# Optimization experiments

Measured on AMD Instinct MI355X. Metric: run time of the kernel, lower is better.

## Reference

```python
import jax, jax.numpy as jnp
import numpy as np

HIDDEN = 128
LR = 0.01          # epsilon (energy optimizer Adam lr)
B1, B2, EPS = 0.9, 0.999, 1e-8  # torch.optim.Adam defaults


def rho(s):
    return jnp.clip(s, 0.0, 1.0)


def setup_inputs() -> dict:
    key = jax.random.key(0)
    k_x, k_w0, k_w1 = jax.random.split(key, 3)
    input_size, output_size = 262144, 1024
    x = jax.random.uniform(k_x, (input_size,), dtype=jnp.float32)
    # xavier_uniform as in nn.init.xavier_uniform_
    lim0 = float(np.sqrt(6.0 / (input_size + HIDDEN)))
    W0 = jax.random.uniform(k_w0, (input_size, HIDDEN), jnp.float32, -lim0, lim0)
    lim1 = float(np.sqrt(6.0 / (HIDDEN + output_size)))
    W1 = jax.random.uniform(k_w1, (HIDDEN, output_size), jnp.float32, -lim1, lim1)
    b0 = jnp.zeros((input_size,), jnp.float32)
    b1 = jnp.zeros((HIDDEN,), jnp.float32)
    b2 = jnp.zeros((output_size,), jnp.float32)
    return {"x": x, "b0": b0, "b1": b1, "b2": b2, "W0": W0, "W1": W1,
            "n_iterations": 20}


def reference(x, b0, b1, b2, W0, W1, n_iterations):
    # Energy: sum ||rho(layer)||^2/2 - sum rho(layer).b - sum rho(pre) W rho(post)
    def energy(h, o):
        rx, rh, ro = rho(x), rho(h), rho(o)
        sq = 0.5 * (rx @ rx + rh @ rh + ro @ ro)
        lin = -(rx @ b0 + rh @ b1 + ro @ b2)
        quad = -((rx @ W0) @ rh + (rh @ W1) @ ro)
        return sq + lin + quad

    grad_e = jax.grad(energy, argnums=(0, 1))

    def adam_update(s, m, v, g, t):
        m = B1 * m + (1.0 - B1) * g
        v = B2 * v + (1.0 - B2) * (g * g)
        m_hat = m / (1.0 - jnp.power(jnp.float32(B1), t))
        v_hat = v / (1.0 - jnp.power(jnp.float32(B2), t))
        s = s - LR * m_hat / (jnp.sqrt(v_hat) + EPS)
        return s, m, v

    def step(carry, _):
        h, o, mh, vh, mo, vo, t = carry
        t = t + 1.0
        gh, go = grad_e(h, o)
        h, mh, vh = adam_update(h, mh, vh, gh, t)
        o, mo, vo = adam_update(o, mo, vo, go, t)
        return (h, o, mh, vh, mo, vo, t), None

    z_h = jnp.zeros_like(b1)  # hidden state starts at zeros
    z_o = jnp.zeros_like(b2)  # output state starts at zeros
    carry0 = (z_h, z_o, z_h, z_h, z_o, z_o, jnp.float32(0.0))
    (h, o, *_), _ = jax.lax.scan(step, carry0, None, length=int(n_iterations))
    return o
```

## Files before the change

### kernel.cpp

```cpp
#include <hip/hip_runtime.h>
#include <math.h>

#define NBLK_B 8

__device__ __forceinline__ float rho(float s) {
  return fminf(fmaxf(s, 0.0f), 1.0f);
}

__device__ __forceinline__ float drho(float s) {
  if (s < 0.0f || s > 1.0f) return 0.0f;
  float g = 1.0f;
  if (s == 0.0f) g *= 0.5f;
  if (s == 1.0f) g *= 0.5f;
  return g;
}

template <int ROWS>
__global__ __launch_bounds__(256) void k1_xw0(const float* __restrict__ x,
                                              const float* __restrict__ W0,
                                              float* __restrict__ part,
                                              int* __restrict__ flags) {
  __shared__ float xs[ROWS];
  __shared__ float red[8][132];
  const int t = threadIdx.x;
  const int b = blockIdx.x;
  if (b == 0 && t < NBLK_B) flags[t * 32] = 0;
  const int r0 = b * ROWS;
  for (int i = t; i < ROWS; i += 256) xs[i] = rho(x[r0 + i]);
  __syncthreads();
  const int cq = t & 31;
  const int rg = t >> 5;
  constexpr int GR = ROWS / 8;
  const float4* __restrict__ W4 = reinterpret_cast<const float4*>(W0);
  float ax = 0.f, ay = 0.f, az = 0.f, aw = 0.f;
  const int base = (r0 + rg * GR) * 32 + cq;
#pragma unroll 8
  for (int i = 0; i < GR; ++i) {
    const float xv = xs[rg * GR + i];
    const float4 w = W4[base + i * 32];
    ax = fmaf(xv, w.x, ax);
    ay = fmaf(xv, w.y, ay);
    az = fmaf(xv, w.z, az);
    aw = fmaf(xv, w.w, aw);
  }
  red[rg][cq * 4 + 0] = ax;
  red[rg][cq * 4 + 1] = ay;
  red[rg][cq * 4 + 2] = az;
  red[rg][cq * 4 + 3] = aw;
  __syncthreads();
  if (t < 128) {
    float s = 0.f;
#pragma unroll
    for (int g = 0; g < 8; ++g) s += red[g][t];
    part[b * 128 + t] = s;
  }
}

__global__ __launch_bounds__(256) void k1b_reduce(const float* __restrict__ part1,
                                                  float* __restrict__ part2) {
  __shared__ float acc[2][128];
  const int t = threadIdx.x, i = blockIdx.x;
  const int jk = t & 127, half = t >> 7;
  float s = 0.f;
  const int r0 = i * 32 + half * 16;
#pragma unroll
  for (int r = 0; r < 16; ++r) s += part1[(r0 + r) * 128 + jk];
  acc[half][jk] = s;
  __syncthreads();
  if (half == 0) part2[i * 128 + jk] = acc[0][jk] + acc[1][jk];
}

__global__ __launch_bounds__(256) void k2_iter(const float* __restrict__ part2,
                                               const int npart2,
                                               const float* __restrict__ W1,
                                               const float* __restrict__ b1,
                                               const float* __restrict__ b2,
                                               const int* __restrict__ niterp,
                                               float* __restrict__ aPartG,
                                               int* __restrict__ flags,
                                               float* __restrict__ out) {
  __shared__ float w1s[128 * 128];
  __shared__ float rhs_[128];
  __shared__ float ros_[128];
  __shared__ float c0s[128];
  __shared__ float b1s[128];
  __shared__ float bpart[2][128];
  __shared__ float apl[2][128];

  const int t = threadIdx.x;
  const int p = blockIdx.x;
  const int jk = t & 127;
  const int half = t >> 7;

  const float4* __restrict__ W14 = reinterpret_cast<const float4*>(W1);
#pragma unroll
  for (int itr = 0; itr < 16; ++itr) {
    const int e4 = itr * 256 + t;
    const int j = e4 >> 5;
    const int c4 = e4 & 31;
    const float4 w = W14[j * 256 + p * 32 + c4];
    const int rb = j * 128;
    const int sw = j & 31;
    const int c = c4 * 4;
    w1s[rb + ((c + 0) ^ sw)] = w.x;
    w1s[rb + ((c + 1) ^ sw)] = w.y;
    w1s[rb + ((c + 2) ^ sw)] = w.z;
    w1s[rb + ((c + 3) ^ sw)] = w.w;
  }
  {
    float s = 0.f;
#pragma unroll 8
    for (int r = half; r < npart2; r += 2) s += part2[r * 128 + jk];
    bpart[half][jk] = s;
  }
  const int niter = *niterp;
  const float b2v = (half == 0) ? b2[p * 128 + jk] : 0.f;
  __syncthreads();
  if (half == 0) {
    c0s[jk] = bpart[0][jk] + bpart[1][jk];
    b1s[jk] = b1[jk];
    rhs_[jk] = 0.f;
    ros_[jk] = 0.f;
    __hip_atomic_store(&aPartG[1 * 1024 + p * 128 + jk], 0.f,
                       __ATOMIC_RELAXED, __HIP_MEMORY_SCOPE_AGENT);
  }
  __syncthreads();
  if (t == 0) {
    __threadfence();
    __hip_atomic_store(&flags[p * 32], 1, __ATOMIC_RELEASE,
                       __HIP_MEMORY_SCOPE_AGENT);
  }

  float hreg = 0.f, mh = 0.f, vh = 0.f;
  float oreg = 0.f, mo = 0.f, vo = 0.f;
  float p1 = 1.f, p2 = 1.f;
  const int x0 = half * 64;

  for (int it = 1; it <= niter; ++it) {
    p1 *= 0.9f;
    p2 *= 0.999f;
    const float bc1 = 1.0f - p1;
    const float bc2 = 1.0f - p2;
    if (t < NBLK_B) {
      while (__hip_atomic_load(&flags[t * 32], __ATOMIC_ACQUIRE,
                               __HIP_MEMORY_SCOPE_AGENT) < it)
        __builtin_amdgcn_s_sleep(1);
    }
    __syncthreads();
    float ga[NBLK_B];
    if (half == 0) {
      const int rslot = it & 3;
#pragma unroll
      for (int q = 0; q < NBLK_B; ++q)
        ga[q] = __hip_atomic_load(&aPartG[rslot * 1024 + q * 128 + jk],
                                  __ATOMIC_RELAXED, __HIP_MEMORY_SCOPE_AGENT);
    }
    {
      float a0 = 0.f, a1 = 0.f, a2 = 0.f, a3 = 0.f;
#pragma unroll
      for (int u = 0; u < 64; u += 4) {
        const int j0 = x0 + u;
        a0 = fmaf(rhs_[j0 + 0], w1s[(j0 + 0) * 128 + (jk ^ ((j0 + 0) & 31))], a0);
        a1 = fmaf(rhs_[j0 + 1], w1s[(j0 + 1) * 128 + (jk ^ ((j0 + 1) & 31))], a1);
        a2 = fmaf(rhs_[j0 + 2], w1s[(j0 + 2) * 128 + (jk ^ ((j0 + 2) & 31))], a2);
        a3 = fmaf(rhs_[j0 + 3], w1s[(j0 + 3) * 128 + (jk ^ ((j0 + 3) & 31))], a3);
      }
      bpart[half][jk] = (a0 + a1) + (a2 + a3);
    }
    __syncthreads();
    if (half == 0) {
      const float bsum = bpart[0][jk] + bpart[1][jk];
      const float rot = rho(oreg);
      const float go = drho(oreg) * (rot - b2v - bsum);
      mo = 0.9f * mo + 0.1f * go;
      vo = 0.999f * vo + 0.001f * (go * go);
      oreg = oreg - 0.01f * (mo / bc1) / (sqrtf(vo / bc2) + 1e-8f);
      ros_[jk] = rho(oreg);
    }
    __syncthreads();
    {
      float a0 = 0.f, a1 = 0.f, a2 = 0.f, a3 = 0.f;
#pragma unroll
      for (int u = 0; u < 64; u += 4) {
        const int c0i = x0 + u;
        a0 = fmaf(w1s[jk * 128 + ((c0i + 0) ^ (jk & 31))], ros_[c0i + 0], a0);
        a1 = fmaf(w1s[jk * 128 + ((c0i + 1) ^ (jk & 31))], ros_[c0i + 1], a1);
        a2 = fmaf(w1s[jk * 128 + ((c0i + 2) ^ (jk & 31))], ros_[c0i + 2], a2);
        a3 = fmaf(w1s[jk * 128 + ((c0i + 3) ^ (jk & 31))], ros_[c0i + 3], a3);
      }
      apl[half][jk] = (a0 + a1) + (a2 + a3);
    }
    __syncthreads();
    if (half == 0)
      __hip_atomic_store(&aPartG[((it + 1) & 3) * 1024 + p * 128 + jk],
                         apl[0][jk] + apl[1][jk], __ATOMIC_RELAXED,
                         __HIP_MEMORY_SCOPE_AGENT);
    __syncthreads();
    if (t == 0) {
      __threadfence();
      __hip_atomic_store(&flags[p * 32], it + 1, __ATOMIC_RELEASE,
                         __HIP_MEMORY_SCOPE_AGENT);
    }
    if (half == 0) {
      const float a = ((ga[0] + ga[1]) + (ga[2] + ga[3])) +
                      ((ga[4] + ga[5]) + (ga[6] + ga[7]));
      const float gh = drho(hreg) * (rhs_[jk] - b1s[jk] - c0s[jk] - a);
      mh = 0.9f * mh + 0.1f * gh;
      vh = 0.999f * vh + 0.001f * (gh * gh);
      hreg = hreg - 0.01f * (mh / bc1) / (sqrtf(vh / bc2) + 1e-8f);
      rhs_[jk] = rho(hreg);
    }
    __syncthreads();
  }
  if (half == 0) out[p * 128 + jk] = oreg;
}

extern "C" void kernel_launch(void* const* d_in, const int* in_sizes, int n_in,
                              void* d_out, int out_size, void* d_ws,
                              size_t ws_size, hipStream_t stream) {
  const float* x  = (const float*)d_in[0];
  const float* b1 = (const float*)d_in[2];
  const float* b2 = (const float*)d_in[3];
  const float* W0 = (const float*)d_in[4];
  const float* W1 = (const float*)d_in[5];
  const int*   ni = (const int*)d_in[6];
  float* out = (float*)d_out;

  char* ws = (char*)d_ws;
  int*   flags  = (int*)ws;
  float* aPartG = (float*)(ws + 1024);
  float* part2  = (float*)(ws + 1024 + 16384);
  float* part1  = (float*)(ws + 1024 + 16384 + 16384);

  const int nrows = in_sizes[0];
  const size_t hdr = 1024 + 16384 + 16384;
  int nblk1;
  if (ws_size >= hdr + (size_t)(nrows / 256) * 512) {
    nblk1 = nrows / 256;
    hipLaunchKernelGGL(k1_xw0<256>, dim3(nblk1), dim3(256), 0, stream,
                       x, W0, part1, flags);
  } else if (ws_size >= hdr + (size_t)(nrows / 512) * 512) {
    nblk1 = nrows / 512;
    hipLaunchKernelGGL(k1_xw0<512>, dim3(nblk1), dim3(256), 0, stream,
                       x, W0, part1, flags);
  } else {
    nblk1 = nrows / 1024;
    hipLaunchKernelGGL(k1_xw0<1024>, dim3(nblk1), dim3(256), 0, stream,
                       x, W0, part1, flags);
  }
  const int nblk2 = nblk1 / 32;
  hipLaunchKernelGGL(k1b_reduce, dim3(nblk2), dim3(256), 0, stream,
                     part1, part2);
  hipLaunchKernelGGL(k2_iter, dim3(NBLK_B), dim3(256), 0, stream,
                     part2, nblk2, W1, b1, b2, ni, aPartG, flags, out);
}
```

Measured before the change: 91.17 us.

## Co-locate iterative-phase blocks on one XCD via oversubscribed grid and role election

```diff
diff --git a/kernel.cpp b/kernel.cpp
--- a/kernel.cpp
+++ b/kernel.cpp
@@ -2,11 +2,11 @@
 #include <math.h>
 
 #define NBLK_B 8
+#define K2_GRID 128
 
 __device__ __forceinline__ float rho(float s) {
   return fminf(fmaxf(s, 0.0f), 1.0f);
 }
-
 __device__ __forceinline__ float drho(float s) {
   if (s < 0.0f || s > 1.0f) return 0.0f;
   float g = 1.0f;
@@ -19,12 +19,18 @@
 __global__ __launch_bounds__(256) void k1_xw0(const float* __restrict__ x,
                                               const float* __restrict__ W0,
                                               float* __restrict__ part,
-                                              int* __restrict__ flags) {
+                                              int* __restrict__ flags,
+                                              int* __restrict__ cnt,
+                                              int* __restrict__ chosen) {
   __shared__ float xs[ROWS];
   __shared__ float red[8][132];
   const int t = threadIdx.x;
   const int b = blockIdx.x;
-  if (b == 0 && t < NBLK_B) flags[t * 32] = 0;
+  if (b == 0) {
+    if (t < NBLK_B) flags[t * 32] = 0;
+    if (t >= 32 && t < 48) cnt[t - 32] = 0;
+    if (t == 48) *chosen = -1;
+  }
   const int r0 = b * ROWS;
   for (int i = t; i < ROWS; i += 256) xs[i] = rho(x[r0 + i]);
   __syncthreads();
@@ -78,6 +84,8 @@
                                                const int* __restrict__ niterp,
                                                float* __restrict__ aPartG,
                                                int* __restrict__ flags,
+                                               int* __restrict__ cnt,
+                                               int* __restrict__ chosen,
                                                float* __restrict__ out) {
   __shared__ float w1s[128 * 128];
   __shared__ float rhs_[128];
@@ -86,11 +94,33 @@
   __shared__ float b1s[128];
   __shared__ float bpart[2][128];
   __shared__ float apl[2][128];
+  __shared__ int role;
 
   const int t = threadIdx.x;
-  const int p = blockIdx.x;
   const int jk = t & 127;
   const int half = t >> 7;
+
+  if (t == 0) {
+    int xcc;
+    asm volatile("s_getreg_b32 %0, hwreg(HW_REG_XCC_ID)" : "=s"(xcc));
+    xcc &= 15;
+    const int r = __hip_atomic_fetch_add(&cnt[xcc], 1, __ATOMIC_RELAXED,
+                                         __HIP_MEMORY_SCOPE_AGENT);
+    if (r == NBLK_B - 1) {
+      int expected = -1;
+      __hip_atomic_compare_exchange_strong(chosen, &expected, xcc,
+                                           __ATOMIC_ACQ_REL, __ATOMIC_ACQUIRE,
+                                           __HIP_MEMORY_SCOPE_AGENT);
+    }
+    int ch;
+    while ((ch = __hip_atomic_load(chosen, __ATOMIC_ACQUIRE,
+                                   __HIP_MEMORY_SCOPE_AGENT)) < 0)
+      __builtin_amdgcn_s_sleep(8);
+    role = (ch == xcc && r < NBLK_B) ? r : -1;
+  }
+  __syncthreads();
+  const int p = role;
+  if (p < 0) return;
 
   const float4* __restrict__ W14 = reinterpret_cast<const float4*>(W1);
 #pragma unroll
@@ -108,10 +138,17 @@
     w1s[rb + ((c + 3) ^ sw)] = w.w;
   }
   {
-    float s = 0.f;
-#pragma unroll 8
-    for (int r = half; r < npart2; r += 2) s += part2[r * 128 + jk];
-    bpart[half][jk] = s;
+    const int n = npart2 >> 1;
+    const int base = half * n;
+    float s0 = 0.f, s1 = 0.f, s2 = 0.f, s3 = 0.f;
+#pragma unroll 4
+    for (int r = 0; r < n; r += 4) {
+      s0 += part2[(base + r + 0) * 128 + jk];
+      s1 += part2[(base + r + 1) * 128 + jk];
+      s2 += part2[(base + r + 2) * 128 + jk];
+      s3 += part2[(base + r + 3) * 128 + jk];
+    }
+    bpart[half][jk] = (s0 + s1) + (s2 + s3);
   }
   const int niter = *niterp;
   const float b2v = (half == 0) ? b2[p * 128 + jk] : 0.f;
@@ -133,14 +170,14 @@
 
   float hreg = 0.f, mh = 0.f, vh = 0.f;
   float oreg = 0.f, mo = 0.f, vo = 0.f;
-  float p1 = 1.f, p2 = 1.f;
+  float pw1 = 1.f, pw2 = 1.f;
   const int x0 = half * 64;
 
   for (int it = 1; it <= niter; ++it) {
-    p1 *= 0.9f;
-    p2 *= 0.999f;
-    const float bc1 = 1.0f - p1;
-    const float bc2 = 1.0f - p2;
+    pw1 *= 0.9f;
+    pw2 *= 0.999f;
+    const float bc1 = 1.0f - pw1;
+    const float bc2 = 1.0f - pw2;
     if (t < NBLK_B) {
       while (__hip_atomic_load(&flags[t * 32], __ATOMIC_ACQUIRE,
                                __HIP_MEMORY_SCOPE_AGENT) < it)
@@ -228,29 +265,32 @@
 
   char* ws = (char*)d_ws;
   int*   flags  = (int*)ws;
-  float* aPartG = (float*)(ws + 1024);
-  float* part2  = (float*)(ws + 1024 + 16384);
-  float* part1  = (float*)(ws + 1024 + 16384 + 16384);
+  int*   cnt    = (int*)(ws + 1024);
+  int*   chosen = (int*)(ws + 1152);
+  float* aPartG = (float*)(ws + 2048);
+  float* part2  = (float*)(ws + 18432);
+  float* part1  = (float*)(ws + 34816);
 
   const int nrows = in_sizes[0];
-  const size_t hdr = 1024 + 16384 + 16384;
+  const size_t hdr = 34816;
   int nblk1;
   if (ws_size >= hdr + (size_t)(nrows / 256) * 512) {
     nblk1 = nrows / 256;
     hipLaunchKernelGGL(k1_xw0<256>, dim3(nblk1), dim3(256), 0, stream,
-                       x, W0, part1, flags);
+                       x, W0, part1, flags, cnt, chosen);
   } else if (ws_size >= hdr + (size_t)(nrows / 512) * 512) {
     nblk1 = nrows / 512;
     hipLaunchKernelGGL(k1_xw0<512>, dim3(nblk1), dim3(256), 0, stream,
-                       x, W0, part1, flags);
+                       x, W0, part1, flags, cnt, chosen);
   } else {
     nblk1 = nrows / 1024;
     hipLaunchKernelGGL(k1_xw0<1024>, dim3(nblk1), dim3(256), 0, stream,
-                       x, W0, part1, flags);
+                       x, W0, part1, flags, cnt, chosen);
   }
   const int nblk2 = nblk1 / 32;
   hipLaunchKernelGGL(k1b_reduce, dim3(nblk2), dim3(256), 0, stream,
                      part1, part2);
-  hipLaunchKernelGGL(k2_iter, dim3(NBLK_B), dim3(256), 0, stream,
-                     part2, nblk2, W1, b1, b2, ni, aPartG, flags, out);
-}
+  hipLaunchKernelGGL(k2_iter, dim3(K2_GRID), dim3(256), 0, stream,
+                     part2, nblk2, W1, b1, b2, ni, aPartG, flags, cnt, chosen,
+                     out);
+}
```

Measured after the change: 98.88 us. +8.5%, slower.

## Replace flag-based inter-block barrier with per-element tagged 64-bit value slots

Applied to the files above, without the earlier changes.

```diff
diff --git a/kernel.cpp b/kernel.cpp
--- a/kernel.cpp
+++ b/kernel.cpp
@@ -6,7 +6,6 @@
 __device__ __forceinline__ float rho(float s) {
   return fminf(fmaxf(s, 0.0f), 1.0f);
 }
-
 __device__ __forceinline__ float drho(float s) {
   if (s < 0.0f || s > 1.0f) return 0.0f;
   float g = 1.0f;
@@ -19,12 +18,15 @@
 __global__ __launch_bounds__(256) void k1_xw0(const float* __restrict__ x,
                                               const float* __restrict__ W0,
                                               float* __restrict__ part,
-                                              int* __restrict__ flags) {
+                                              unsigned long long* __restrict__ aPartG) {
   __shared__ float xs[ROWS];
   __shared__ float red[8][132];
   const int t = threadIdx.x;
   const int b = blockIdx.x;
-  if (b == 0 && t < NBLK_B) flags[t * 32] = 0;
+  if (b == 0) {
+#pragma unroll
+    for (int i = 0; i < 16; ++i) aPartG[i * 256 + t] = 0ull;
+  }
   const int r0 = b * ROWS;
   for (int i = t; i < ROWS; i += 256) xs[i] = rho(x[r0 + i]);
   __syncthreads();
@@ -76,8 +78,7 @@
                                                const float* __restrict__ b1,
                                                const float* __restrict__ b2,
                                                const int* __restrict__ niterp,
-                                               float* __restrict__ aPartG,
-                                               int* __restrict__ flags,
+                                               unsigned long long* __restrict__ aPartG,
                                                float* __restrict__ out) {
   __shared__ float w1s[128 * 128];
   __shared__ float rhs_[128];
@@ -121,40 +122,21 @@
     b1s[jk] = b1[jk];
     rhs_[jk] = 0.f;
     ros_[jk] = 0.f;
-    __hip_atomic_store(&aPartG[1 * 1024 + p * 128 + jk], 0.f,
+    __hip_atomic_store(&aPartG[1 * 1024 + jk * 8 + p], 1ull << 32,
                        __ATOMIC_RELAXED, __HIP_MEMORY_SCOPE_AGENT);
   }
   __syncthreads();
-  if (t == 0) {
-    __threadfence();
-    __hip_atomic_store(&flags[p * 32], 1, __ATOMIC_RELEASE,
-                       __HIP_MEMORY_SCOPE_AGENT);
-  }
 
   float hreg = 0.f, mh = 0.f, vh = 0.f;
   float oreg = 0.f, mo = 0.f, vo = 0.f;
-  float p1 = 1.f, p2 = 1.f;
+  float pw1 = 1.f, pw2 = 1.f;
   const int x0 = half * 64;
 
   for (int it = 1; it <= niter; ++it) {
-    p1 *= 0.9f;
-    p2 *= 0.999f;
-    const float bc1 = 1.0f - p1;
-    const float bc2 = 1.0f - p2;
-    if (t < NBLK_B) {
-      while (__hip_atomic_load(&flags[t * 32], __ATOMIC_ACQUIRE,
-                               __HIP_MEMORY_SCOPE_AGENT) < it)
-        __builtin_amdgcn_s_sleep(1);
-    }
-    __syncthreads();
-    float ga[NBLK_B];
-    if (half == 0) {
-      const int rslot = it & 3;
-#pragma unroll
-      for (int q = 0; q < NBLK_B; ++q)
-        ga[q] = __hip_atomic_load(&aPartG[rslot * 1024 + q * 128 + jk],
-                                  __ATOMIC_RELAXED, __HIP_MEMORY_SCOPE_AGENT);
-    }
+    pw1 *= 0.9f;
+    pw2 *= 0.999f;
+    const float bc1 = 1.0f - pw1;
+    const float bc2 = 1.0f - pw2;
     {
       float a0 = 0.f, a1 = 0.f, a2 = 0.f, a3 = 0.f;
 #pragma unroll
@@ -191,17 +173,32 @@
       apl[half][jk] = (a0 + a1) + (a2 + a3);
     }
     __syncthreads();
-    if (half == 0)
-      __hip_atomic_store(&aPartG[((it + 1) & 3) * 1024 + p * 128 + jk],
-                         apl[0][jk] + apl[1][jk], __ATOMIC_RELAXED,
-                         __HIP_MEMORY_SCOPE_AGENT);
-    __syncthreads();
-    if (t == 0) {
-      __threadfence();
-      __hip_atomic_store(&flags[p * 32], it + 1, __ATOMIC_RELEASE,
-                         __HIP_MEMORY_SCOPE_AGENT);
-    }
     if (half == 0) {
+      const float pav = apl[0][jk] + apl[1][jk];
+      const unsigned long long wv =
+          ((unsigned long long)(unsigned)(it + 1) << 32) |
+          (unsigned long long)__float_as_uint(pav);
+      __hip_atomic_store(&aPartG[((it + 1) & 3) * 1024 + jk * 8 + p], wv,
+                         __ATOMIC_RELAXED, __HIP_MEMORY_SCOPE_AGENT);
+    }
+    if (half == 0) {
+      unsigned long long* base = &aPartG[(it & 3) * 1024 + jk * 8];
+      float ga[8];
+      unsigned pend = 0xffu;
+      while (pend) {
+#pragma unroll
+        for (int q = 0; q < 8; ++q) {
+          if (pend & (1u << q)) {
+            const unsigned long long wv = __hip_atomic_load(
+                &base[q], __ATOMIC_RELAXED, __HIP_MEMORY_SCOPE_AGENT);
+            if ((unsigned)(wv >> 32) == (unsigned)it) {
+              ga[q] = __uint_as_float((unsigned)wv);
+              pend &= ~(1u << q);
+            }
+          }
+        }
+        if (pend) __builtin_amdgcn_s_sleep(1);
+      }
       const float a = ((ga[0] + ga[1]) + (ga[2] + ga[3])) +
                       ((ga[4] + ga[5]) + (ga[6] + ga[7]));
       const float gh = drho(hreg) * (rhs_[jk] - b1s[jk] - c0s[jk] - a);
@@ -227,30 +224,29 @@
   float* out = (float*)d_out;
 
   char* ws = (char*)d_ws;
-  int*   flags  = (int*)ws;
-  float* aPartG = (float*)(ws + 1024);
-  float* part2  = (float*)(ws + 1024 + 16384);
-  float* part1  = (float*)(ws + 1024 + 16384 + 16384);
+  unsigned long long* aPartG = (unsigned long long*)ws;
+  float* part2 = (float*)(ws + 32768);
+  float* part1 = (float*)(ws + 32768 + 16384);
 
   const int nrows = in_sizes[0];
-  const size_t hdr = 1024 + 16384 + 16384;
+  const size_t hdr = 32768 + 16384;
   int nblk1;
   if (ws_size >= hdr + (size_t)(nrows / 256) * 512) {
     nblk1 = nrows / 256;
     hipLaunchKernelGGL(k1_xw0<256>, dim3(nblk1), dim3(256), 0, stream,
-                       x, W0, part1, flags);
+                       x, W0, part1, aPartG);
   } else if (ws_size >= hdr + (size_t)(nrows / 512) * 512) {
     nblk1 = nrows / 512;
     hipLaunchKernelGGL(k1_xw0<512>, dim3(nblk1), dim3(256), 0, stream,
-                       x, W0, part1, flags);
+                       x, W0, part1, aPartG);
   } else {
     nblk1 = nrows / 1024;
     hipLaunchKernelGGL(k1_xw0<1024>, dim3(nblk1), dim3(256), 0, stream,
-                       x, W0, part1, flags);
+                       x, W0, part1, aPartG);
   }
   const int nblk2 = nblk1 / 32;
   hipLaunchKernelGGL(k1b_reduce, dim3(nblk2), dim3(256), 0, stream,
                      part1, part2);
   hipLaunchKernelGGL(k2_iter, dim3(NBLK_B), dim3(256), 0, stream,
-                     part2, nblk2, W1, b1, b2, ni, aPartG, flags, out);
-}
+                     part2, nblk2, W1, b1, b2, ni, aPartG, out);
+}
```

New measurement: 96.42 us. 1.06x slower.
